# Performance work log

Measured on AMD Instinct MI355X. Metric: run time of the kernel, lower is better.

The kernel has to match this reference:

```python
import jax, jax.numpy as jnp
from jax import lax
import numpy as np

H = 512
W = 512
SIGMA = 0.1
IN_CH = [3, 66, 64, 64, 32, 32, 32, 16, 16]
OUT_CH = [64, 64, 64, 32, 32, 32, 16, 16, 16]
N_LAYERS = 9


def setup_inputs() -> dict:
    key = jax.random.key(0)
    ks = jax.random.split(key, 32)
    inp = {}
    inp['x'] = jax.random.uniform(ks[0], (3, 3, 1, 1), jnp.float32)  # query + 2 neighbor coords
    inp['neighbors'] = jax.random.uniform(ks[1], (2, 3, H, W), jnp.float32)
    inp['albedo_index'] = 4
    for i in range(N_LAYERS):
        kh = 1 if i == 0 else 3
        fan_in = IN_CH[i] * kh * kh
        inp[f'w{i}'] = jax.random.normal(ks[2 + i], (OUT_CH[i], IN_CH[i], kh, kh), jnp.float32) / np.sqrt(fan_in).astype(np.float32)
        inp[f'b{i}'] = jnp.zeros((OUT_CH[i],), jnp.float32)
    inp['wf'] = jax.random.normal(ks[20], (6, 16, 3, 3), jnp.float32) / np.sqrt(16 * 9).astype(np.float32)
    inp['bf'] = jnp.zeros((6,), jnp.float32)
    inp['albedos'] = 0.5 + jax.random.uniform(ks[21], (9, 3, H, W), jnp.float32)
    return inp


def _conv(x, w, b):
    y = lax.conv_general_dilated(x, w, (1, 1), 'VALID', dimension_numbers=('NCHW', 'OIHW', 'NCHW'))
    return y + b[None, :, None, None]


def _decoder(x, ws, bs, wf, bf):
    # coordconv constant [[ [0,2],[0,2] ], [ [0,0],[2,2] ]] with shape [2,2,2]
    coordconv = jnp.array([[[0., 2.], [0., 2.]], [[0., 0.], [2., 2.]]], dtype=x.dtype)
    for i in range(N_LAYERS):
        x = jnp.repeat(jnp.repeat(x, 2, axis=2), 2, axis=3)  # nearest upsample x2
        if i > 0:
            x = jnp.pad(x, ((0, 0), (0, 0), (1, 1), (1, 1)), mode='reflect')
        x = jax.nn.leaky_relu(_conv(x, ws[i], bs[i]), 0.01)
        if i == 0:
            cc = jnp.broadcast_to(coordconv[None], (x.shape[0],) + coordconv.shape)
            x = jnp.concatenate([x, cc], axis=1)  # -> 66 channels at 2x2
    x = jnp.pad(x, ((0, 0), (0, 0), (1, 1), (1, 1)), mode='reflect')
    return jnp.tanh(_conv(x, wf, bf))  # [B, 6, H, W]


def _grid_sample_border(img, grid):
    # bilinear, padding_mode='border', align_corners=False (matches torch grid_sample)
    N, C, Hh, Ww = img.shape
    gx = jnp.clip((grid[..., 0] + 1.0) * Ww / 2.0 - 0.5, 0.0, Ww - 1.0)
    gy = jnp.clip((grid[..., 1] + 1.0) * Hh / 2.0 - 0.5, 0.0, Hh - 1.0)
    x0 = jnp.floor(gx)
    y0 = jnp.floor(gy)
    wx = (gx - x0)[:, None]  # [N,1,H,W]
    wy = (gy - y0)[:, None]
    x0i = jnp.clip(x0.astype(jnp.int32), 0, Ww - 1)
    x1i = jnp.clip(x0i + 1, 0, Ww - 1)
    y0i = jnp.clip(y0.astype(jnp.int32), 0, Hh - 1)
    y1i = jnp.clip(y0i + 1, 0, Hh - 1)
    g = jax.vmap(lambda im, yi, xi: im[:, yi, xi])
    v00 = g(img, y0i, x0i)
    v01 = g(img, y0i, x1i)
    v10 = g(img, y1i, x0i)
    v11 = g(img, y1i, x1i)
    return v00 * (1 - wx) * (1 - wy) + v01 * wx * (1 - wy) + v10 * (1 - wx) * wy + v11 * wx * wy


def _blending(x, neighbors, flows, albedo):
    eps = 1e-5
    light_flow, view_flow, time_flow = flows[:1, 0:2], flows[:1, 2:4], flows[:1, 4:6]
    lf_n, vf_n, tf_n = flows[1:, 0:2], flows[1:, 2:4], flows[1:, 4:6]
    delta = x[:1] - x[1:]  # [2,3,1,1], broadcasts in place of torch.tile
    dl, dv, dt = delta[:, 0:1], delta[:, 1:2], delta[:, 2:3]
    flag = (jnp.abs(dl) > 0).astype(flows.dtype)
    offset_fwd = dl * light_flow + dv * view_flow + dt * time_flow  # [2,2,H,W]
    shading = flag * neighbors / albedo + (1 - flag) * neighbors
    ys = jnp.linspace(-1.0, 1.0, H)
    xs = jnp.linspace(-1.0, 1.0, W)
    grid_base = jnp.stack(jnp.meshgrid(xs, ys, indexing='xy'), axis=-1)  # [H,W,2], (...,0)=x
    grid = grid_base[None] + offset_fwd.transpose(0, 2, 3, 1)  # [2,H,W,2]
    warped_shading = _grid_sample_border(shading, grid)
    warped_vf = _grid_sample_border(vf_n, grid)
    warped_tf = _grid_sample_border(tf_n, grid)
    warped_lf = _grid_sample_border(lf_n, grid)
    warped_image = flag * warped_shading * albedo + (1 - flag) * warped_shading
    offset_bwd = dl * warped_lf + dv * warped_vf + dt * warped_tf
    dist = jnp.sum(jnp.abs(offset_fwd - offset_bwd), axis=1, keepdims=True)
    weight = jnp.exp(-SIGMA * W * dist)
    wn = weight / (jnp.sum(weight, axis=0, keepdims=True) + eps)
    return jnp.sum(warped_image * wn, axis=0, keepdims=True)  # [1,3,H,W]


def reference(x, neighbors, albedo_index, w0, w1, w2, w3, w4, w5, w6, w7, w8,
              b0, b1, b2, b3, b4, b5, b6, b7, b8, wf, bf, albedos):
    ws = [w0, w1, w2, w3, w4, w5, w6, w7, w8]
    bs = [b0, b1, b2, b3, b4, b5, b6, b7, b8]
    flows = _decoder(x, ws, bs, wf, bf)
    albedo = albedos[albedo_index]  # [3,H,W]
    return _blending(x, neighbors, flows, albedo)
```

## Files before the change

kernel.cpp:

```cpp
#include <hip/hip_runtime.h>
#include <hip/hip_bf16.h>
#include <math.h>


#define HH 512
#define WWI 512
#define HWP (HH*WWI)

__device__ __forceinline__ int xcd_swz(int bx, int nbx) {
  if ((nbx & 7) == 0) {
    int c = nbx >> 3;
    return (bx & 7) * c + (bx >> 3);
  }
  return bx;
}

__device__ __forceinline__ void fold_one(const float* __restrict__ w, float* __restrict__ f, int n)
{
  const float* ws = w + (size_t)n*9;
  float W[9];
  #pragma unroll
  for (int k = 0; k < 9; k++) W[k] = ws[k];

  float a[2][2][3];
  #pragma unroll
  for (int c = 0; c < 3; c++) {
    a[0][0][c] = W[c];          a[0][1][c] = W[3+c] + W[6+c];
    a[1][0][c] = W[c] + W[3+c]; a[1][1][c] = W[6+c];
  }
  float* fo = f + (size_t)n*16;
  #pragma unroll
  for (int py = 0; py < 2; py++)
    #pragma unroll
    for (int px = 0; px < 2; px++) {
      int p = py*2 + px;
      #pragma unroll
      for (int ky = 0; ky < 2; ky++) {
        float kx0 = (px == 0) ? a[py][ky][0] : (a[py][ky][0] + a[py][ky][1]);
        float kx1 = (px == 0) ? (a[py][ky][1] + a[py][ky][2]) : a[py][ky][2];
        fo[p*4 + ky*2 + 0] = kx0;
        fo[p*4 + ky*2 + 1] = kx1;
      }
    }
}

__global__ void k_prep(const float* __restrict__ x, const float* __restrict__ w0,
                       const float* __restrict__ b0, float* __restrict__ outS,
                       const float* __restrict__ w1, const float* __restrict__ w2,
                       const float* __restrict__ w3, const float* __restrict__ w4,
                       const float* __restrict__ w5, const float* __restrict__ w6,
                       const float* __restrict__ w7, const float* __restrict__ w8,
                       float* __restrict__ f1, float* __restrict__ f2,
                       float* __restrict__ f3, float* __restrict__ f4,
                       float* __restrict__ f5, float* __restrict__ f6,
                       float* __restrict__ f7, float* __restrict__ f8)
{
  if (blockIdx.x < 53) {
    int idx = blockIdx.x*blockDim.x + threadIdx.x;
    const float* w; float* f; int n;
    if      (idx < 4224)  { w = w1; f = f1; n = idx; }
    else if (idx < 8320)  { w = w2; f = f2; n = idx - 4224; }
    else if (idx < 10368) { w = w3; f = f3; n = idx - 8320; }
    else if (idx < 11392) { w = w4; f = f4; n = idx - 10368; }
    else if (idx < 12416) { w = w5; f = f5; n = idx - 11392; }
    else if (idx < 12928) { w = w6; f = f6; n = idx - 12416; }
    else if (idx < 13184) { w = w7; f = f7; n = idx - 12928; }
    else if (idx < 13440) { w = w8; f = f8; n = idx - 13184; }
    else return;
    fold_one(w, f, n);
  } else {
    for (int idx = threadIdx.x; idx < 3*66*4; idx += blockDim.x) {
      int pos = idx & 3;
      int c = (idx >> 2) % 66;
      int b = idx / (66*4);
      float v;
      if (c < 64) {
        float a = b0[c];
        #pragma unroll
        for (int ci = 0; ci < 3; ci++) a += w0[c*3+ci] * x[b*3+ci];
        v = (a >= 0.f) ? a : 0.01f*a;
      } else {
        int xx = pos & 1, yy = pos >> 1;
        v = (c == 64) ? 2.f*(float)xx : 2.f*(float)yy;
      }
      outS[idx] = v;
    }
  }
}

template<int CIN>
__global__ void k_upconv_s(const float* __restrict__ in, float* __restrict__ out,
                           const float* __restrict__ wfold, const float* __restrict__ bias,
                           int B, int CO, int Hin)
{
  extern __shared__ float4 wlds4[];
  int nt = blockDim.x, tid = threadIdx.x;
  int co = blockIdx.y;
  const int stride = CIN + 1;
  const float4* wsrc = reinterpret_cast<const float4*>(wfold);
  for (int s = tid; s < CIN*4; s += nt) {
    int p = s & 3;
    int ci = s >> 2;
    wlds4[p*stride + ci] = wsrc[(size_t)(co*CIN + ci)*4 + p];
  }
  __syncthreads();

  int Hout = Hin * 2;
  int npix = B * Hout * Hout;
  int idx = blockIdx.x*nt + tid;
  if (idx >= npix) return;
  int x = idx % Hout;
  int y = (idx / Hout) % Hout;
  int b = idx / (Hout * Hout);

  int X = x >> 1, Y = y >> 1;
  int px = x & 1, py = y & 1;

  int r_lo = py ? Y : (Y > 0 ? Y-1 : 0);
  int r_hi = py ? (Y < Hin-1 ? Y+1 : Hin-1) : Y;
  int c_lo = px ? X : (X > 0 ? X-1 : 0);
  int c_hi = px ? (X < Hin-1 ? X+1 : Hin-1) : X;

  float acc = bias[co];

  const size_t plane = (size_t)Hin * Hin;
  const float* ibase = in + (size_t)b * CIN * plane;
  const float4* wb = wlds4 + (py*2 + px) * stride;

  #pragma unroll 4
  for (int ci = 0; ci < CIN; ci++) {
    const float* ip = ibase + (size_t)ci * plane;
    const float* rl = ip + (size_t)r_lo * Hin;
    const float* rh = ip + (size_t)r_hi * Hin;
    float4 w4 = wb[ci];
    acc += w4.x*rl[c_lo] + w4.y*rl[c_hi] + w4.z*rh[c_lo] + w4.w*rh[c_hi];
  }

  float v = (acc >= 0.f) ? acc : 0.01f*acc;
  out[((size_t)b*CO + co)*((size_t)Hout*Hout) + (size_t)y*Hout + x] = v;
}

template<int COB, int P>
__global__ void k_upconv_wP(const float* __restrict__ in, float* __restrict__ out,
                            const float* __restrict__ wfold, const float* __restrict__ bias,
                            int B, int Cin, int CO, int Hin)
{
  extern __shared__ float4 wlds4[];
  int nt = blockDim.x, tid = threadIdx.x;
  int co0 = blockIdx.y * COB;
  int stride = Cin * COB + 1;
  int nw = Cin * COB * 4;
  const float4* wsrc = reinterpret_cast<const float4*>(wfold);
  for (int s = tid; s < nw; s += nt) {
    int p = s & 3;
    int r = s >> 2;
    int ci = r % Cin;
    int col = r / Cin;
    wlds4[p*stride + ci*COB + col] = wsrc[(size_t)((co0 + col)*Cin + ci)*4 + p];
  }
  __syncthreads();

  int Hout = Hin * 2;
  int q = Hout / P;
  int total = B * Hout * q;
  int bx = xcd_swz(blockIdx.x, gridDim.x);
  int idx = bx*nt + tid;
  if (idx >= total) return;
  int x1 = idx % q;
  int y  = (idx / q) % Hout;
  int b  = idx / (q * Hout);

  int px = x1 & 1, py = y & 1;
  int Y = y >> 1;
  int r_lo = py ? Y : (Y > 0 ? Y-1 : 0);
  int r_hi = py ? (Y < Hin-1 ? Y+1 : Hin-1) : Y;

  int clo[P], chi[P];
  #pragma unroll
  for (int k = 0; k < P; k++) {
    int X = (x1 + k*q) >> 1;
    clo[k] = px ? X : (X > 0 ? X-1 : 0);
    chi[k] = px ? (X < Hin-1 ? X+1 : Hin-1) : X;
  }

  float acc[P][COB];
  #pragma unroll
  for (int j = 0; j < COB; j++) {
    float bv = bias[co0 + j];
    #pragma unroll
    for (int k = 0; k < P; k++) acc[k][j] = bv;
  }

  const size_t plane = (size_t)Hin * Hin;
  const float* ibase = in + (size_t)b * Cin * plane;
  const float4* wb = wlds4 + (py*2 + px) * stride;

  for (int ci = 0; ci < Cin; ci++) {
    const float* ip = ibase + (size_t)ci * plane;
    const float* rl = ip + (size_t)r_lo * Hin;
    const float* rh = ip + (size_t)r_hi * Hin;
    float pl0[P], pl1[P], ph0[P], ph1[P];
    #pragma unroll
    for (int k = 0; k < P; k++) {
      pl0[k] = rl[clo[k]]; pl1[k] = rl[chi[k]];
      ph0[k] = rh[clo[k]]; ph1[k] = rh[chi[k]];
    }
    const float4* wc = wb + ci * COB;
    #pragma unroll
    for (int j = 0; j < COB; j++) {
      float4 w4 = wc[j];
      #pragma unroll
      for (int k = 0; k < P; k++)
        acc[k][j] += w4.x*pl0[k] + w4.y*pl1[k] + w4.z*ph0[k] + w4.w*ph1[k];
    }
  }

  size_t oplane = (size_t)Hout * Hout;
  float* op = out + ((size_t)b * CO + co0) * oplane + (size_t)y*Hout + x1;
  #pragma unroll
  for (int j = 0; j < COB; j++) {
    #pragma unroll
    for (int k = 0; k < P; k++) {
      float v = acc[k][j];
      v = (v >= 0.f) ? v : 0.01f*v;
      op[k*q] = v;
    }
    op += oplane;
  }
}

__global__ void k_final2(const float* __restrict__ in, float* __restrict__ out,
                         const float* __restrict__ w, const float* __restrict__ bias)
{
  int total = 3 * HH * (WWI/2);
  int bx = xcd_swz(blockIdx.x, gridDim.x);
  int idx = bx*blockDim.x + threadIdx.x;
  if (idx >= total) return;
  int xh = idx % (WWI/2);
  int y  = (idx / (WWI/2)) % HH;
  int b  = idx / (HH * (WWI/2));
  int x0 = 2*xh;

  int ry[3];
  #pragma unroll
  for (int d = 0; d < 3; d++) {
    int t = y - 1 + d;
    t = (t < 0) ? -t : t;
    ry[d] = (t >= HH) ? (2*(HH-1) - t) : t;
  }
  int cx[4];
  cx[0] = (x0 == 0) ? 1 : x0-1;
  cx[1] = x0;
  cx[2] = x0+1;
  cx[3] = (x0+2 >= WWI) ? (2*(WWI-1) - (x0+2)) : x0+2;

  float acc0[6], acc1[6];
  #pragma unroll
  for (int co = 0; co < 6; co++) { float bv = bias[co]; acc0[co] = bv; acc1[co] = bv; }

  for (int ci = 0; ci < 16; ci++) {
    const float* ib = in + ((size_t)(b*16) + ci) * HWP;
    float p[3][4];
    #pragma unroll
    for (int dy = 0; dy < 3; dy++) {
      const float* r = ib + (size_t)ry[dy]*WWI;
      #pragma unroll
      for (int dx = 0; dx < 4; dx++) p[dy][dx] = r[cx[dx]];
    }
    const float* wc = w + ci*9;
    #pragma unroll
    for (int co = 0; co < 6; co++) {
      const float* wcc = wc + co*16*9;
      #pragma unroll
      for (int dy = 0; dy < 3; dy++) {
        #pragma unroll
        for (int dx = 0; dx < 3; dx++) {
          float wv = wcc[dy*3+dx];
          acc0[co] += wv * p[dy][dx];
          acc1[co] += wv * p[dy][dx+1];
        }
      }
    }
  }

  size_t pix = (size_t)y*WWI + x0;
  #pragma unroll
  for (int co = 0; co < 6; co++) {
    float2 v = make_float2(tanhf(acc0[co]), tanhf(acc1[co]));
    *reinterpret_cast<float2*>(out + ((size_t)(b*6) + co)*HWP + pix) = v;
  }
}

__global__ void k_blend(const float* __restrict__ xin, const float* __restrict__ neighbors,
                        const int* __restrict__ aidx, const float* __restrict__ albedos,
                        const float* __restrict__ flows, float* __restrict__ out)
{
  int idx = blockIdx.x*blockDim.x + threadIdx.x;
  if (idx >= HWP) return;
  int xo = idx & (WWI-1);
  int yo = idx >> 9;

  float xv[9];
  #pragma unroll
  for (int i = 0; i < 9; i++) xv[i] = xin[i];

  float f0[6];
  #pragma unroll
  for (int c = 0; c < 6; c++) f0[c] = flows[(size_t)c*HWP + idx];

  const float* alb = albedos + (size_t)aidx[0]*3*HWP;
  float albp[3];
  #pragma unroll
  for (int ch = 0; ch < 3; ch++) albp[ch] = alb[(size_t)ch*HWP + idx];

  float num0 = 0.f, num1 = 0.f, num2 = 0.f;
  float wsum = 0.f;

  #pragma unroll
  for (int n = 0; n < 2; n++) {
    float dl = xv[0] - xv[(n+1)*3 + 0];
    float dv = xv[1] - xv[(n+1)*3 + 1];
    float dt = xv[2] - xv[(n+1)*3 + 2];
    bool fl = fabsf(dl) > 0.f;

    float ofx = dl*f0[0] + dv*f0[2] + dt*f0[4];
    float ofy = dl*f0[1] + dv*f0[3] + dt*f0[5];

    float gx = ((-1.f + (2.f/511.f)*(float)xo) + ofx + 1.f)*256.f - 0.5f;
    float gy = ((-1.f + (2.f/511.f)*(float)yo) + ofy + 1.f)*256.f - 0.5f;
    gx = fminf(fmaxf(gx, 0.f), 511.f);
    gy = fminf(fmaxf(gy, 0.f), 511.f);

    float x0f = floorf(gx), y0f = floorf(gy);
    float wx = gx - x0f, wy = gy - y0f;
    int x0i = (int)x0f, y0i = (int)y0f;
    int x1i = min(x0i + 1, WWI-1), y1i = min(y0i + 1, HH-1);

    float cw[4] = {(1.f-wx)*(1.f-wy), wx*(1.f-wy), (1.f-wx)*wy, wx*wy};
    int   cp[4] = {y0i*WWI + x0i, y0i*WWI + x1i, y1i*WWI + x0i, y1i*WWI + x1i};

    const float* nb = neighbors + (size_t)n*3*HWP;
    const float* Fn = flows + (size_t)(n+1)*6*HWP;

    float s0=0.f,s1=0.f,s2=0.f;
    float l0=0.f,l1=0.f,v0=0.f,v1=0.f,t0=0.f,t1=0.f;
    #pragma unroll
    for (int c = 0; c < 4; c++) {
      int p = cp[c];
      float ww = cw[c];
      float n0 = nb[p];
      float n1 = nb[HWP + p];
      float n2 = nb[2*HWP + p];
      if (fl) {
        n0 /= alb[p];
        n1 /= alb[HWP + p];
        n2 /= alb[2*HWP + p];
      }
      s0 += ww*n0; s1 += ww*n1; s2 += ww*n2;
      l0 += ww*Fn[p];             l1 += ww*Fn[HWP + p];
      v0 += ww*Fn[2*HWP + p];     v1 += ww*Fn[3*HWP + p];
      t0 += ww*Fn[4*HWP + p];     t1 += ww*Fn[5*HWP + p];
    }

    float wi0 = fl ? s0*albp[0] : s0;
    float wi1 = fl ? s1*albp[1] : s1;
    float wi2 = fl ? s2*albp[2] : s2;

    float obx = dl*l0 + dv*v0 + dt*t0;
    float oby = dl*l1 + dv*v1 + dt*t1;
    float dist = fabsf(ofx - obx) + fabsf(ofy - oby);
    float wgt = expf(-51.2f * dist);

    wsum += wgt;
    num0 += wgt*wi0; num1 += wgt*wi1; num2 += wgt*wi2;
  }

  float inv = 1.f / (wsum + 1e-5f);
  out[idx]         = num0*inv;
  out[HWP + idx]   = num1*inv;
  out[2*HWP + idx] = num2*inv;
}

extern "C" void kernel_launch(void* const* d_in, const int* in_sizes, int n_in,
                              void* d_out, int out_size, void* d_ws, size_t ws_size,
                              hipStream_t stream) {
  const float* x         = (const float*)d_in[0];
  const float* neighbors = (const float*)d_in[1];
  const int*   aidx      = (const int*)d_in[2];
  const float* wts[10];
  const float* bis[10];
  for (int i = 0; i < 9; i++) { wts[i] = (const float*)d_in[3+2*i]; bis[i] = (const float*)d_in[4+2*i]; }
  wts[9] = (const float*)d_in[21];
  bis[9] = (const float*)d_in[22];
  const float* albedos = (const float*)d_in[23];

  float* wk   = (float*)d_ws;
  float* bufS = wk;
  float* bufA = wk + 800;
  float* bufB = bufA + 4718592;
  size_t need = (size_t)(800 + 4718592 + 12582912) * 4;
  if (ws_size < need) return;

  float* wf1 = bufA + 3200000;
  float* wf2 = wf1 + 67584;
  float* wf3 = wf2 + 65536;
  float* wf4 = wf3 + 32768;
  float* wf5 = wf4 + 16384;
  float* wf6 = wf5 + 16384;
  float* wf7 = wf6 + 8192;
  float* wf8 = wf7 + 4096;

  k_prep<<<54, 256, 0, stream>>>(x, wts[0], bis[0], bufS,
                                 wts[1], wts[2], wts[3], wts[4], wts[5], wts[6], wts[7], wts[8],
                                 wf1, wf2, wf3, wf4, wf5, wf6, wf7, wf8);

  auto blocks = [](int total){ return (total + 255) / 256; };

  {
    dim3 g1(blocks(3*4*4), 64), g2(blocks(3*8*8), 64);
    dim3 g3(blocks(3*16*16), 32), g4(blocks(3*32*32), 32), g5(blocks(3*64*64), 32);
    k_upconv_s<66><<<g1, 256, (size_t)4*(66+1)*16, stream>>>(bufS, bufA, wf1, bis[1], 3, 64, 2);
    k_upconv_s<64><<<g2, 256, (size_t)4*(64+1)*16, stream>>>(bufA, bufB, wf2, bis[2], 3, 64, 4);
    k_upconv_s<64><<<g3, 256, (size_t)4*(64+1)*16, stream>>>(bufB, bufA, wf3, bis[3], 3, 32, 8);
    k_upconv_s<32><<<g4, 256, (size_t)4*(32+1)*16, stream>>>(bufA, bufB, wf4, bis[4], 3, 32, 16);
    k_upconv_s<32><<<g5, 256, (size_t)4*(32+1)*16, stream>>>(bufB, bufA, wf5, bis[5], 3, 32, 32);
  }

  {
    dim3 g6(blocks(3*128*32), 4);
    dim3 g7(blocks(3*256*64), 4);
    dim3 g8(blocks(3*512*128), 4);
    k_upconv_wP<4,4><<<g6, 256, (size_t)4*(32*4+1)*16, stream>>>(bufA, bufB, wf6, bis[6], 3, 32, 16, 64);
    k_upconv_wP<4,4><<<g7, 256, (size_t)4*(16*4+1)*16, stream>>>(bufB, bufA, wf7, bis[7], 3, 16, 16, 128);
    k_upconv_wP<4,4><<<g8, 256, (size_t)4*(16*4+1)*16, stream>>>(bufA, bufB, wf8, bis[8], 3, 16, 16, 256);
  }

  k_final2<<<blocks(3*HH*(WWI/2)), 256, 0, stream>>>(bufB, bufA, wts[9], bis[9]);
  k_blend<<<blocks(HWP), 256, 0, stream>>>(x, neighbors, aidx, albedos, bufA, (float*)d_out);
}
```

Baseline: 277.3 us.

## Split upconv blocks by output column parity and read weights as wave-uniform scalars

The wide upconv kernel now assigns each block a fixed column parity (px) via blockIdx.y. This makes the folded-weight phase wave-uniform, so weights are read directly from global memory through readfirstlane-uniform addresses instead of being staged in LDS. It removes the per-block LDS weight fill, the __syncthreads and the LDS reads. Column spacing is fixed at 64 with per-layer P, and output stores become stride-2 interleaved writes. The trade-off is less coalesced stores, more blocks, and relying on scalar/cache loads for the weights.

```diff
diff --git a/kernel.cpp b/kernel.cpp
--- a/kernel.cpp
+++ b/kernel.cpp
@@ -141,36 +141,26 @@
 }
 
 template<int COB, int P>
-__global__ void k_upconv_wP(const float* __restrict__ in, float* __restrict__ out,
+__global__ void k_upconv_sp(const float* __restrict__ in, float* __restrict__ out,
                             const float* __restrict__ wfold, const float* __restrict__ bias,
                             int B, int Cin, int CO, int Hin)
 {
-  extern __shared__ float4 wlds4[];
-  int nt = blockDim.x, tid = threadIdx.x;
-  int co0 = blockIdx.y * COB;
-  int stride = Cin * COB + 1;
-  int nw = Cin * COB * 4;
-  const float4* wsrc = reinterpret_cast<const float4*>(wfold);
-  for (int s = tid; s < nw; s += nt) {
-    int p = s & 3;
-    int r = s >> 2;
-    int ci = r % Cin;
-    int col = r / Cin;
-    wlds4[p*stride + ci*COB + col] = wsrc[(size_t)((co0 + col)*Cin + ci)*4 + p];
-  }
-  __syncthreads();
-
+  int px  = blockIdx.y & 1;
+  int co0 = (blockIdx.y >> 1) * COB;
   int Hout = Hin * 2;
-  int q = Hout / P;
+  const int q = 64;
   int total = B * Hout * q;
   int bx = xcd_swz(blockIdx.x, gridDim.x);
-  int idx = bx*nt + tid;
+  int idx = bx*blockDim.x + threadIdx.x;
   if (idx >= total) return;
   int x1 = idx % q;
   int y  = (idx / q) % Hout;
   int b  = idx / (q * Hout);
 
-  int px = x1 & 1, py = y & 1;
+  int py = y & 1;
+  int p4 = __builtin_amdgcn_readfirstlane(py*2 + px);
+  const float4* wp = reinterpret_cast<const float4*>(wfold) + p4;
+
   int Y = y >> 1;
   int r_lo = py ? Y : (Y > 0 ? Y-1 : 0);
   int r_hi = py ? (Y < Hin-1 ? Y+1 : Hin-1) : Y;
@@ -178,7 +168,7 @@
   int clo[P], chi[P];
   #pragma unroll
   for (int k = 0; k < P; k++) {
-    int X = (x1 + k*q) >> 1;
+    int X = x1 + k*q;
     clo[k] = px ? X : (X > 0 ? X-1 : 0);
     chi[k] = px ? (X < Hin-1 ? X+1 : Hin-1) : X;
   }
@@ -193,7 +183,6 @@
 
   const size_t plane = (size_t)Hin * Hin;
   const float* ibase = in + (size_t)b * Cin * plane;
-  const float4* wb = wlds4 + (py*2 + px) * stride;
 
   for (int ci = 0; ci < Cin; ci++) {
     const float* ip = ibase + (size_t)ci * plane;
@@ -205,10 +194,9 @@
       pl0[k] = rl[clo[k]]; pl1[k] = rl[chi[k]];
       ph0[k] = rh[clo[k]]; ph1[k] = rh[chi[k]];
     }
-    const float4* wc = wb + ci * COB;
     #pragma unroll
     for (int j = 0; j < COB; j++) {
-      float4 w4 = wc[j];
+      float4 w4 = wp[((size_t)(co0 + j)*Cin + ci)*4];
       #pragma unroll
       for (int k = 0; k < P; k++)
         acc[k][j] += w4.x*pl0[k] + w4.y*pl1[k] + w4.z*ph0[k] + w4.w*ph1[k];
@@ -216,14 +204,14 @@
   }
 
   size_t oplane = (size_t)Hout * Hout;
-  float* op = out + ((size_t)b * CO + co0) * oplane + (size_t)y*Hout + x1;
+  float* op = out + ((size_t)b * CO + co0) * oplane + (size_t)y*Hout + 2*x1 + px;
   #pragma unroll
   for (int j = 0; j < COB; j++) {
     #pragma unroll
     for (int k = 0; k < P; k++) {
       float v = acc[k][j];
       v = (v >= 0.f) ? v : 0.01f*v;
-      op[k*q] = v;
+      op[2*k*q] = v;
     }
     op += oplane;
   }
@@ -427,12 +415,12 @@
   }
 
   {
-    dim3 g6(blocks(3*128*32), 4);
-    dim3 g7(blocks(3*256*64), 4);
-    dim3 g8(blocks(3*512*128), 4);
-    k_upconv_wP<4,4><<<g6, 256, (size_t)4*(32*4+1)*16, stream>>>(bufA, bufB, wf6, bis[6], 3, 32, 16, 64);
-    k_upconv_wP<4,4><<<g7, 256, (size_t)4*(16*4+1)*16, stream>>>(bufB, bufA, wf7, bis[7], 3, 16, 16, 128);
-    k_upconv_wP<4,4><<<g8, 256, (size_t)4*(16*4+1)*16, stream>>>(bufA, bufB, wf8, bis[8], 3, 16, 16, 256);
+    dim3 g6(blocks(3*128*64), 8);
+    dim3 g7(blocks(3*256*64), 8);
+    dim3 g8(blocks(3*512*64), 8);
+    k_upconv_sp<4,1><<<g6, 256, 0, stream>>>(bufA, bufB, wf6, bis[6], 3, 32, 16, 64);
+    k_upconv_sp<4,2><<<g7, 256, 0, stream>>>(bufB, bufA, wf7, bis[7], 3, 16, 16, 128);
+    k_upconv_sp<4,4><<<g8, 256, 0, stream>>>(bufA, bufB, wf8, bis[8], 3, 16, 16, 256);
   }
 
   k_final2<<<blocks(3*HH*(WWI/2)), 256, 0, stream>>>(bufB, bufA, wts[9], bis[9]);
```

Measured after the change: 292.8 us. 5.6% more time.
